# Optimization experiments

Measured on AMD Instinct MI355X. Metric: run time of the kernel, lower is better.

The kernel has to match this reference:

```python
import jax, jax.numpy as jnp
import numpy as np


def _quantum_act(x, act_w):
    # LearnedQuantumActivation, eval mode (no phase noise): softmax-weighted mix of 9 activations
    w = jax.nn.softmax(act_w)
    mish = x * jnp.tanh(jax.nn.softplus(x))
    return (w[0] * jax.nn.sigmoid(x) + w[1] * jax.nn.elu(x) + w[2] * jnp.tanh(x)
            + w[3] * jax.nn.relu(x) + w[4] * jax.nn.silu(x)
            + w[5] * jax.nn.gelu(x, approximate=False) + w[6] * jax.nn.selu(x)
            + w[7] * mish + w[8] * x)


def setup_inputs() -> dict:
    B, D, U, N = 1024, 1024, 2048, 4      # batch, input_dim, max_units, num_branches
    M, MD, O, H = 2048, 1024, 512, 64     # memory_size, memory_dim, output_dim, critic hidden
    key = jax.random.key(0)
    ks = jax.random.split(key, 16)
    g = lambda k, shape, s=0.02: jax.random.normal(k, shape, dtype=jnp.float32) * s
    return {
        "x": jax.random.normal(ks[0], (B, D), dtype=jnp.float32),
        "w": g(ks[1], (D, U, N)),
        "b": jnp.zeros((U, N), jnp.float32),
        "gate_w": g(ks[2], (D, N)), "gate_b": jnp.zeros((N,), jnp.float32),
        "act_w": jnp.ones((9,), jnp.float32),
        "mask": jnp.ones((U,), jnp.float32),          # neuron_mask, initial_units == max_units
        "mem": g(ks[3], (M, MD), 0.05),
        "att_w": g(ks[4], (U, M)), "att_b": jnp.zeros((M,), jnp.float32),
        "write_w": g(ks[5], (U, MD)), "write_b": jnp.zeros((MD,), jnp.float32),
        "update_gate": jnp.full((M,), 0.5, jnp.float32),
        "out_w": g(ks[6], (U, O)), "out_b": jnp.zeros((O,), jnp.float32),
        "cw1": g(ks[7], (MD, H // 2)), "cb1": jnp.zeros((H // 2,), jnp.float32),
        "cw2": g(ks[8], (O, H // 2)), "cb2": jnp.zeros((H // 2,), jnp.float32),
        "cw3": g(ks[9], (U, H // 2)), "cb3": jnp.zeros((H // 2,), jnp.float32),
        "cw4": g(ks[10], (3 * (H // 2), H)), "cb4": jnp.zeros((H,), jnp.float32),
        "cw5": g(ks[11], (H, 2)), "cb5": jnp.zeros((2,), jnp.float32),
        "meta_threshold": jnp.float32(0.5),
    }


def reference(x, w, b, gate_w, gate_b, act_w, mask, mem, att_w, att_b,
              write_w, write_b, update_gate, out_w, out_b,
              cw1, cb1, cw2, cb2, cw3, cb3, cw4, cb4, cw5, cb5, meta_threshold):
    # Dendritic plastic dense: per-branch projections mixed by a learned softmax branch gate
    pre = jnp.einsum('bi,iun->bun', x, w) + b               # (B, U, N)
    gate = jax.nn.softmax(x @ gate_w + gate_b, axis=-1)     # (B, N)
    hidden = _quantum_act(jnp.einsum('bun,bn->bu', pre, gate), act_w) * mask  # (B, U)
    # Episodic memory read + write (write is returned instead of in-place assign)
    read_att = jax.nn.softmax(hidden @ att_w + att_b, axis=-1)  # (B, M)
    read = read_att @ mem                                       # (B, MD)
    cand = jnp.tanh(hidden @ write_w + write_b)                 # (B, MD)
    u = (jnp.mean(read_att, axis=0) * update_gate)[:, None]     # (M, 1)
    new_mem = mem * (1.0 - u) + u * jnp.mean(cand, axis=0)      # (M, MD)
    # Prediction head
    preds = hidden @ out_w + out_b                              # (B, O)
    # Metacognitive critic gating
    mf = jax.nn.relu(read @ cw1 + cb1)
    pf = jax.nn.relu(preds @ cw2 + cb2)
    hf = jax.nn.relu(hidden @ cw3 + cb3)
    fused = jax.nn.relu(jnp.concatenate([mf, pf, hf], axis=-1) @ cw4 + cb4)
    outs = fused @ cw5 + cb5
    gating = jax.nn.sigmoid(outs[:, 0:1] - meta_threshold)
    return (preds * gating, new_mem)
```

## Files before the change

### kernel.cpp

```cpp
#include <hip/hip_runtime.h>
#include <hip/hip_bf16.h>
#include <math.h>

typedef __attribute__((ext_vector_type(4))) float f32x4;
typedef __attribute__((ext_vector_type(2))) float f32x2;
typedef __attribute__((ext_vector_type(8))) short s16x8;
typedef __attribute__((ext_vector_type(4))) short s16x4;
typedef __hip_bfloat16 bf16;

#define MB (1024ull*1024ull)
#define GATE_OFF    (0ull)
#define ACTW_OFF    (16ull*1024)
#define U_OFF       (20ull*1024)
#define CMEAN_OFF   (28ull*1024)
#define PART_OFF    (64ull*1024)
#define HIDDEN_OFF  (1ull*MB)
#define RATT_OFF    (5ull*MB)
#define CAND_OFF    (9ull*MB)
#define PREDS_OFF   (11ull*MB)
#define READ_OFF    (13ull*MB)
#define XBF_OFF     (17ull*MB)
#define WT_OFF      (19ull*MB)
#define CATT_OFF    (35ull*MB)
#define MEMT_OFF    (49ull*MB)
#define READ2_OFF   WT_OFF

__device__ __forceinline__ short f2bf_s(float f) {
    bf16 h = __float2bfloat16(f);
    return *reinterpret_cast<short*>(&h);
}

__device__ __forceinline__ void async_load16(const bf16* g, short* l) {
    __builtin_amdgcn_global_load_lds((const __attribute__((address_space(1))) void*)g,
                                     (__attribute__((address_space(3))) void*)l, 16, 0, 0);
}

__device__ __forceinline__ float fast_tanh(float x) {
    float e2x = __expf(2.f * x);
    return 1.f - 2.f / (e2x + 1.f);
}

__device__ __forceinline__ float qact(float x, const float* w) {
    float ex  = __expf(x);
    float r1  = 1.f / (1.f + ex);
    float sig = 1.f - r1;
    float em1 = ex - 1.f;
    float elu = x > 0.f ? x : em1;
    float e2x = ex * ex;
    float th  = 1.f - 2.f / (e2x + 1.f);
    float rel = fmaxf(x, 0.f);
    float silu = x * sig;
    float u   = 0.7978845608028654f * (x + 0.044715f * x * x * x);
    float e2u = __expf(2.f * u);
    float gel = x * (1.f - 1.f / (e2u + 1.f));
    float sel = 1.0507009873554805f * (x > 0.f ? x : 1.6732632423543772f * em1);
    float t   = 1.f + ex;
    float t2  = t * t;
    float mish = x * (1.f - 2.f / (t2 + 1.f));
    return w[0]*sig + w[1]*elu + w[2]*th + w[3]*rel + w[4]*silu
         + w[5]*gel + w[6]*sel + w[7]*mish + w[8]*x;
}

__device__ __forceinline__ void do_transpose(const float* __restrict__ in,
                                             bf16* __restrict__ out, int R, int C,
                                             int bx, int by, int t, short* tile) {
    int k0 = by*64, n0 = bx*64;
    int i = t & 31, half = t >> 5;
    #pragma unroll
    for (int r = 0; r < 8; r++) {
        int k = half + r*8;
        f32x2 v = *reinterpret_cast<const f32x2*>(&in[(size_t)(k0 + k)*C + n0 + i*2]);
        tile[(i*2 + 0)*66 + k] = f2bf_s(v[0]);
        tile[(i*2 + 1)*66 + k] = f2bf_s(v[1]);
    }
    __syncthreads();
    int kp = t & 31, nrow = t >> 5;
    #pragma unroll
    for (int jj = 0; jj < 8; jj++) {
        int n = nrow + jj*8;
        unsigned lo = (unsigned short)tile[n*66 + kp*2];
        unsigned hi = (unsigned short)tile[n*66 + kp*2 + 1];
        *reinterpret_cast<unsigned*>(&out[(size_t)(n0 + n)*R + k0 + kp*2]) = lo | (hi << 16);
    }
}

__global__ __launch_bounds__(256) void k_prepass(
        const float* __restrict__ x, bf16* __restrict__ xbf,
        const float* __restrict__ gw, const float* __restrict__ gb,
        const float* __restrict__ aw_in,
        float* __restrict__ gate, float* __restrict__ actw,
        const float* __restrict__ w_, bf16* __restrict__ wT,
        const float* __restrict__ att_w, const float* __restrict__ write_w,
        const float* __restrict__ out_w, bf16* __restrict__ catT,
        const float* __restrict__ mem, bf16* __restrict__ memT,
        float* __restrict__ zbase) {
    __shared__ short tile[64*66];
    int blk = blockIdx.x, t = threadIdx.x;
    if (blk < 2048) {
        do_transpose(w_, wT, 1024, 8192, blk & 127, blk >> 7, t, tile);
    } else if (blk < 3072) {
        int rel = blk - 2048;
        do_transpose(att_w, catT, 2048, 2048, rel & 31, rel >> 5, t, tile);
    } else if (blk < 3584) {
        int rel = blk - 3072;
        do_transpose(write_w, catT + 2048ull*2048, 2048, 1024, rel & 15, rel >> 4, t, tile);
    } else if (blk < 3840) {
        int rel = blk - 3584;
        do_transpose(out_w, catT + 3072ull*2048, 2048, 512, rel & 7, rel >> 3, t, tile);
    } else if (blk < 4352) {
        int rel = blk - 3840;
        do_transpose(mem, memT, 2048, 1024, rel & 15, rel >> 4, t, tile);
    } else if (blk < 5376) {
        int i = (blk - 4352)*256 + t;
        f32x4 v = ((const f32x4*)x)[i];
        s16x4 o;
        #pragma unroll
        for (int j = 0; j < 4; j++) o[j] = f2bf_s(v[j]);
        ((s16x4*)xbf)[i] = o;
        if (blk == 4352 && t == 64) {
            float a[9]; float m = -1e30f;
            for (int i2 = 0; i2 < 9; i2++) { a[i2] = aw_in[i2]; m = fmaxf(m, a[i2]); }
            float ss = 0.f;
            for (int i2 = 0; i2 < 9; i2++) { a[i2] = __expf(a[i2]-m); ss += a[i2]; }
            float inv = 1.f / ss;
            for (int i2 = 0; i2 < 9; i2++) actw[i2] = a[i2]*inv;
        }
    } else if (blk < 6400) {
        int b = blk - 5376, w = t >> 6, lane = t & 63;
        __shared__ float l[4];
        float s = 0.f;
        for (int k = lane; k < 1024; k += 64)
            s += x[(size_t)b*1024 + k] * gw[k*4 + w];
        #pragma unroll
        for (int off = 32; off; off >>= 1) s += __shfl_xor(s, off);
        if (lane == 0) l[w] = s + gb[w];
        __syncthreads();
        if (t == 0) {
            float m = fmaxf(fmaxf(l[0], l[1]), fmaxf(l[2], l[3]));
            float e0 = __expf(l[0]-m), e1 = __expf(l[1]-m), e2 = __expf(l[2]-m), e3 = __expf(l[3]-m);
            float inv = 1.f / (e0+e1+e2+e3);
            gate[b*4+0] = e0*inv; gate[b*4+1] = e1*inv;
            gate[b*4+2] = e2*inv; gate[b*4+3] = e3*inv;
        }
    } else {
        int idx = (blk - 6400)*256 + t;
        ((f32x4*)zbase)[idx] = (f32x4){0.f, 0.f, 0.f, 0.f};
    }
}

template <int TM>
union SMemT {
    struct { short a[3][TM*32]; short b[3][128*32]; } tl;
    float z[TM*32];
};

template <int MODE, int TM>
__device__ __forceinline__ void gemm_core(
        int bx, int by, int bz, SMemT<TM>& sm,
        const bf16* __restrict__ A, const bf16* __restrict__ Bt,
        int K, int lda, int ldb, int kOffset,
        const float* __restrict__ bias, const float* __restrict__ bias2,
        const float* __restrict__ bias3,
        float* __restrict__ outF, float* __restrict__ outF2,
        bf16* __restrict__ outH, bf16* __restrict__ outH2,
        const float* __restrict__ gate, const float* __restrict__ actw,
        const float* __restrict__ mask, int outStride) {
    constexpr int MI = TM / 32;
    int t = threadIdx.x, lane = t & 63;
    int rowBase = by * TM, colBase = bx * 128;
    int lm = lane & 15, lq = lane >> 4;
    int w = t >> 6;
    int qm = (w >> 1) * (TM/2), qn = (w & 1) * 64;

    A  += (size_t)kOffset * bz;
    Bt += (size_t)kOffset * bz;

    f32x4 acc[MI][4];
    #pragma unroll
    for (int i = 0; i < MI; i++)
        #pragma unroll
        for (int j = 0; j < 4; j++) acc[i][j] = (f32x4){0.f, 0.f, 0.f, 0.f};

    int cb0 = w*128 + lane, cb1 = cb0 + 64;
    int rb0 = cb0 >> 2, kb0 = ((cb0 & 3) ^ ((rb0 >> 1) & 3)) * 8;
    int rb1 = cb1 >> 2, kb1 = ((cb1 & 3) ^ ((rb1 >> 1) & 3)) * 8;
    int ca0 = (TM == 128) ? (w*128 + lane) : (w*64 + lane);
    int ra0 = ca0 >> 2, ka0 = ((ca0 & 3) ^ ((ra0 >> 1) & 3)) * 8;
    int ca1 = ca0 + 64;
    int ra1 = ca1 >> 2, ka1 = ((ca1 & 3) ^ ((ra1 >> 1) & 3)) * 8;

    auto issueLoads = [&](int k0, int ib) {
        short* bA = sm.tl.a[ib];
        short* bB = sm.tl.b[ib];
        async_load16(A + (size_t)(rowBase + ra0)*lda + k0 + ka0,
                     bA + ((TM == 128) ? w*1024 : w*512));
        if (TM == 128)
            async_load16(A + (size_t)(rowBase + ra1)*lda + k0 + ka1, bA + w*1024 + 512);
        async_load16(Bt + (size_t)(colBase + rb0)*ldb + k0 + kb0, bB + w*1024);
        async_load16(Bt + (size_t)(colBase + rb1)*ldb + k0 + kb1, bB + w*1024 + 512);
    };

    issueLoads(0, 0);
    if (32 < K) issueLoads(32, 1);
    int ib = 0;
    for (int k0 = 0; k0 < K; k0 += 32) {
        if (k0 + 32 < K) {
            if (TM == 128) asm volatile("s_waitcnt vmcnt(4)" ::: "memory");
            else           asm volatile("s_waitcnt vmcnt(3)" ::: "memory");
        } else {
            asm volatile("s_waitcnt vmcnt(0)" ::: "memory");
        }
        __builtin_amdgcn_sched_barrier(0);
        __builtin_amdgcn_s_barrier();
        __builtin_amdgcn_sched_barrier(0);
        int ibn = ib + 2; if (ibn >= 3) ibn -= 3;
        if (k0 + 64 < K) issueLoads(k0 + 64, ibn);
        const short* cA = sm.tl.a[ib];
        const short* cB = sm.tl.b[ib];
        s16x8 af[MI], bfr[4];
        #pragma unroll
        for (int mi = 0; mi < MI; mi++) {
            int r = qm + mi*16 + lm;
            af[mi] = *reinterpret_cast<const s16x8*>(cA + r*32 + ((lq ^ ((r >> 1) & 3)) * 8));
        }
        #pragma unroll
        for (int ni = 0; ni < 4; ni++) {
            int r = qn + ni*16 + lm;
            bfr[ni] = *reinterpret_cast<const s16x8*>(cB + r*32 + ((lq ^ ((r >> 1) & 3)) * 8));
        }
        #pragma unroll
        for (int mi = 0; mi < MI; mi++)
            #pragma unroll
            for (int ni = 0; ni < 4; ni++)
                acc[mi][ni] = __builtin_amdgcn_mfma_f32_16x16x32_bf16(af[mi], bfr[ni], acc[mi][ni], 0, 0, 0);
        ib += 1; if (ib >= 3) ib = 0;
    }

    if (MODE == 4) {
        __syncthreads();
        #pragma unroll
        for (int mi = 0; mi < MI; mi++) {
            int rowl0 = qm + mi*16 + lq*4;
            #pragma unroll
            for (int ni = 0; ni < 4; ni++) {
                int col = colBase + qn + ni*16 + lm;
                int n = col & 3;
                float bb = bias[col];
                f32x4 v = acc[mi][ni];
                #pragma unroll
                for (int r = 0; r < 4; r++) v[r] = (v[r] + bb) * gate[(rowBase + rowl0 + r)*4 + n];
                #pragma unroll
                for (int r = 0; r < 4; r++) v[r] += __shfl_xor(v[r], 1);
                #pragma unroll
                for (int r = 0; r < 4; r++) v[r] += __shfl_xor(v[r], 2);
                if ((lane & 3) == 0) {
                    int ul = ((w & 1) << 4) + ni*4 + (lm >> 2);
                    #pragma unroll
                    for (int r = 0; r < 4; r++)
                        sm.z[(rowl0 + r)*32 + ul] = v[r];
                }
            }
        }
        __syncthreads();
        float aw[9];
        #pragma unroll
        for (int i = 0; i < 9; i++) aw[i] = actw[i];
        int u0 = colBase >> 2;
        #pragma unroll
        for (int i = 0; i < TM/8; i++) {
            int idx = t + i*256;
            int row = idx >> 5, ul = idx & 31;
            int ug = u0 + ul;
            float zz = sm.z[idx];
            outH[(size_t)(rowBase + row)*outStride + ug] = __float2bfloat16(qact(zz, aw) * mask[ug]);
        }
    } else if (MODE == 5) {
        #pragma unroll
        for (int mi = 0; mi < MI; mi++) {
            int row0 = rowBase + qm + mi*16 + lq*4;
            #pragma unroll
            for (int ni = 0; ni < 4; ni++) {
                int col = colBase + qn + ni*16 + lm;
                if (col < 2048) {
                    float bb = bias[col];
                    #pragma unroll
                    for (int r = 0; r < 4; r++)
                        outH[(size_t)(row0 + r)*2048 + col] = __float2bfloat16(acc[mi][ni][r] + bb);
                } else if (col < 3072) {
                    int c = col - 2048;
                    float bb = bias2[c];
                    #pragma unroll
                    for (int r = 0; r < 4; r++)
                        outH2[(size_t)(row0 + r)*1024 + c] = __float2bfloat16(fast_tanh(acc[mi][ni][r] + bb));
                } else {
                    int c = col - 3072;
                    float bb = bias3[c];
                    #pragma unroll
                    for (int r = 0; r < 4; r++)
                        outF[(size_t)(row0 + r)*512 + c] = acc[mi][ni][r] + bb;
                }
            }
        }
    } else {
        float* of = bz ? (outF2 + (size_t)(bz - 1) * 1048576) : outF;
        #pragma unroll
        for (int mi = 0; mi < MI; mi++) {
            int row0 = rowBase + qm + mi*16 + lq*4;
            #pragma unroll
            for (int ni = 0; ni < 4; ni++) {
                int col = colBase + qn + ni*16 + lm;
                #pragma unroll
                for (int r = 0; r < 4; r++)
                    of[(size_t)(row0 + r)*outStride + col] = acc[mi][ni][r];
            }
        }
    }
}

template <int MODE, int TM>
__global__ __launch_bounds__(256, 2) void gemm_bt(
        const bf16* __restrict__ A, const bf16* __restrict__ Bt,
        int K, int lda, int ldb, int kOffset,
        const float* __restrict__ bias, const float* __restrict__ bias2,
        const float* __restrict__ bias3,
        float* __restrict__ outF, float* __restrict__ outF2,
        bf16* __restrict__ outH, bf16* __restrict__ outH2,
        const float* __restrict__ gate, const float* __restrict__ actw,
        const float* __restrict__ mask, int outStride) {
    __shared__ __align__(16) SMemT<TM> sm;
    gemm_core<MODE, TM>(blockIdx.x, blockIdx.y, blockIdx.z, sm,
                        A, Bt, K, lda, ldb, kOffset, bias, bias2, bias3,
                        outF, outF2, outH, outH2, gate, actw, mask, outStride);
}

__global__ __launch_bounds__(256) void k_softmax(bf16* __restrict__ ratt) {
    int b = blockIdx.x, t = threadIdx.x, w = t >> 6, lane = t & 63;
    __shared__ float red[8];
    bf16* row = ratt + (size_t)b*2048;
    float v[8];
    float mx = -1e30f;
    #pragma unroll
    for (int j = 0; j < 8; j++) {
        v[j] = __bfloat162float(row[t + j*256]);
        mx = fmaxf(mx, v[j]);
    }
    #pragma unroll
    for (int off = 32; off; off >>= 1) mx = fmaxf(mx, __shfl_xor(mx, off));
    if (lane == 0) red[w] = mx;
    __syncthreads();
    mx = fmaxf(fmaxf(red[0], red[1]), fmaxf(red[2], red[3]));
    float s = 0.f;
    #pragma unroll
    for (int j = 0; j < 8; j++) { v[j] = __expf(v[j] - mx); s += v[j]; }
    #pragma unroll
    for (int off = 32; off; off >>= 1) s += __shfl_xor(s, off);
    if (lane == 0) red[4 + w] = s;
    __syncthreads();
    float inv = 1.f / (red[4] + red[5] + red[6] + red[7]);
    #pragma unroll
    for (int j = 0; j < 8; j++)
        row[t + j*256] = __float2bfloat16(v[j] * inv);
}

__global__ __launch_bounds__(256, 2) void k_g5x(
        const bf16* __restrict__ ratt, const bf16* __restrict__ memT,
        const bf16* __restrict__ cand,
        float* __restrict__ readv, float* __restrict__ readv2,
        const float* __restrict__ update_gate,
        float* __restrict__ u, float* __restrict__ cmean) {
    __shared__ __align__(16) SMemT<64> sm;
    int bid = blockIdx.x, t = threadIdx.x;
    if (bid < 512) {
        int bx = bid & 7, by = (bid >> 3) & 15, bz = bid >> 7;
        gemm_core<3, 64>(bx, by, bz, sm, ratt, memT, 512, 2048, 2048, 512,
                         nullptr, nullptr, nullptr, readv, readv2, nullptr, nullptr,
                         nullptr, nullptr, nullptr, 1024);
    } else {
        int rel = bid - 512;
        int ct = rel % 12, rc = rel / 12;
        int col = ct*256 + t;
        const bf16* src; int stride, c;
        if (ct < 8) { src = ratt; stride = 2048; c = col; }
        else        { src = cand; stride = 1024; c = col - 2048; }
        float s = 0.f;
        int r0 = rc*128;
        for (int r2 = 0; r2 < 128; r2++)
            s += __bfloat162float(src[(size_t)(r0 + r2)*stride + c]);
        if (ct < 8) atomicAdd(&u[col], s * (update_gate[col] * (1.f/1024.f)));
        else        atomicAdd(&cmean[col - 2048], s * (1.f/1024.f));
    }
}

__global__ __launch_bounds__(256) void k_fin(
        const float* __restrict__ readv, const float* __restrict__ readv2,
        const float* __restrict__ preds, const bf16* __restrict__ hidden,
        const float* cw1, const float* cb1, const float* cw2, const float* cb2,
        const float* cw3, const float* cb3, const float* cw4, const float* cb4,
        const float* cw5, const float* cb5, const float* thr,
        float* __restrict__ out0,
        const float* __restrict__ mem, const float* __restrict__ u,
        const float* __restrict__ cmean, float* __restrict__ out1) {
    __shared__ __align__(16) float sx[2*1024];
    __shared__ __align__(16) float sp[2*512];
    __shared__ __align__(16) short sh[2*2048];
    __shared__ __align__(16) f32x4 part[2][32][8];
    __shared__ float feat[2][96];
    __shared__ float fused[2][64];
    __shared__ float gsh[2];
    int bid = blockIdx.x, t = threadIdx.x;
    if (bid >= 512) {
        int idx = (bid - 512)*256 + t;
        int m = idx >> 8, d4 = idx & 255;
        float um = u[m];
        f32x4 m4 = ((const f32x4*)mem)[idx];
        f32x4 c4 = ((const f32x4*)cmean)[d4];
        f32x4 o;
        #pragma unroll
        for (int j = 0; j < 4; j++) o[j] = m4[j] * (1.f - um) + um * c4[j];
        ((f32x4*)out1)[idx] = o;
        return;
    }
    int b0 = bid * 2;
    int j4 = t & 7, kg = t >> 3;

    {
        const f32x4* r0 = (const f32x4*)(readv  + (size_t)b0*1024);
        const f32x4* r1 = (const f32x4*)(readv2 + (size_t)b0*1024);
        const f32x4* r2 = (const f32x4*)(readv2 + 1048576 + (size_t)b0*1024);
        const f32x4* r3 = (const f32x4*)(readv2 + 2097152 + (size_t)b0*1024);
        ((f32x4*)sx)[t]       = r0[t] + r1[t] + r2[t] + r3[t];
        ((f32x4*)sx)[t + 256] = r0[t + 256] + r1[t + 256] + r2[t + 256] + r3[t + 256];
    }
    ((f32x4*)sp)[t]       = ((const f32x4*)(preds + (size_t)b0*512))[t];
    ((s16x8*)sh)[t]       = ((const s16x8*)(hidden + (size_t)b0*2048))[t];
    ((s16x8*)sh)[t + 256] = ((const s16x8*)(hidden + (size_t)b0*2048))[t + 256];
    __syncthreads();

    {
        const f32x4* wv = (const f32x4*)cw1;
        f32x4 a0 = (f32x4){0,0,0,0}, a1 = (f32x4){0,0,0,0};
        int k0 = kg*32;
        #pragma unroll 4
        for (int k = k0; k < k0 + 32; k++) {
            f32x4 wq = wv[k*8 + j4];
            a0 += sx[k] * wq;
            a1 += sx[1024 + k] * wq;
        }
        part[0][kg][j4] = a0; part[1][kg][j4] = a1;
    }
    __syncthreads();
    if (t < 64) {
        int r = t >> 5, f = t & 31;
        float s = 0.f;
        #pragma unroll
        for (int i = 0; i < 32; i++) s += part[r][i][f >> 2][f & 3];
        feat[r][f] = fmaxf(s + cb1[f], 0.f);
    }
    __syncthreads();
    {
        const f32x4* wv = (const f32x4*)cw2;
        f32x4 a0 = (f32x4){0,0,0,0}, a1 = (f32x4){0,0,0,0};
        int k0 = kg*16;
        #pragma unroll 4
        for (int k = k0; k < k0 + 16; k++) {
            f32x4 wq = wv[k*8 + j4];
            a0 += sp[k] * wq;
            a1 += sp[512 + k] * wq;
        }
        part[0][kg][j4] = a0; part[1][kg][j4] = a1;
    }
    __syncthreads();
    if (t < 64) {
        int r = t >> 5, f = t & 31;
        float s = 0.f;
        #pragma unroll
        for (int i = 0; i < 32; i++) s += part[r][i][f >> 2][f & 3];
        feat[r][32 + f] = fmaxf(s + cb2[f], 0.f);
    }
    __syncthreads();
    {
        const f32x4* wv = (const f32x4*)cw3;
        f32x4 a0 = (f32x4){0,0,0,0}, a1 = (f32x4){0,0,0,0};
        int k0 = kg*64;
        #pragma unroll 4
        for (int k = k0; k < k0 + 64; k++) {
            f32x4 wq = wv[k*8 + j4];
            float h0 = __bfloat162float(*reinterpret_cast<const bf16*>(&sh[k]));
            float h1 = __bfloat162float(*reinterpret_cast<const bf16*>(&sh[2048 + k]));
            a0 += h0 * wq;
            a1 += h1 * wq;
        }
        part[0][kg][j4] = a0; part[1][kg][j4] = a1;
    }
    __syncthreads();
    if (t < 64) {
        int r = t >> 5, f = t & 31;
        float s = 0.f;
        #pragma unroll
        for (int i = 0; i < 32; i++) s += part[r][i][f >> 2][f & 3];
        feat[r][64 + f] = fmaxf(s + cb3[f], 0.f);
    }
    __syncthreads();
    if (t < 128) {
        int r = t >> 6, uu = t & 63;
        float s = 0.f;
        #pragma unroll 8
        for (int k = 0; k < 96; k++) s += feat[r][k] * cw4[k*64 + uu];
        fused[r][uu] = fmaxf(s + cb4[uu], 0.f);
    }
    __syncthreads();
    if (t < 128) {
        int r = t >> 6, lane = t & 63;
        float v = fused[r][lane] * cw5[lane*2];
        #pragma unroll
        for (int off = 32; off; off >>= 1) v += __shfl_xor(v, off);
        if (lane == 0)
            gsh[r] = 1.f / (1.f + __expf(-(v + cb5[0] - thr[0])));
    }
    __syncthreads();
    #pragma unroll
    for (int idx = t; idx < 1024; idx += 256) {
        int r = idx >> 9, o = idx & 511;
        out0[(size_t)(b0 + r)*512 + o] = sp[r*512 + o] * gsh[r];
    }
}

extern "C" void kernel_launch(void* const* d_in, const int* in_sizes, int n_in,
                              void* d_out, int out_size, void* d_ws, size_t ws_size,
                              hipStream_t stream) {
    const float* x        = (const float*)d_in[0];
    const float* w_       = (const float*)d_in[1];
    const float* b_bias   = (const float*)d_in[2];
    const float* gate_w   = (const float*)d_in[3];
    const float* gate_b   = (const float*)d_in[4];
    const float* act_w    = (const float*)d_in[5];
    const float* mask     = (const float*)d_in[6];
    const float* mem      = (const float*)d_in[7];
    const float* att_w    = (const float*)d_in[8];
    const float* att_b    = (const float*)d_in[9];
    const float* write_w  = (const float*)d_in[10];
    const float* write_b  = (const float*)d_in[11];
    const float* upd_gate = (const float*)d_in[12];
    const float* out_w    = (const float*)d_in[13];
    const float* out_b    = (const float*)d_in[14];
    const float* cw1 = (const float*)d_in[15]; const float* cb1 = (const float*)d_in[16];
    const float* cw2 = (const float*)d_in[17]; const float* cb2 = (const float*)d_in[18];
    const float* cw3 = (const float*)d_in[19]; const float* cb3 = (const float*)d_in[20];
    const float* cw4 = (const float*)d_in[21]; const float* cb4 = (const float*)d_in[22];
    const float* cw5 = (const float*)d_in[23]; const float* cb5 = (const float*)d_in[24];
    const float* thr = (const float*)d_in[25];

    char* ws = (char*)d_ws;
    float* gate   = (float*)(ws + GATE_OFF);
    float* actw   = (float*)(ws + ACTW_OFF);
    float* uvec   = (float*)(ws + U_OFF);
    float* cmean  = (float*)(ws + CMEAN_OFF);
    bf16*  hidden = (bf16*)(ws + HIDDEN_OFF);
    bf16*  ratt   = (bf16*)(ws + RATT_OFF);
    bf16*  cand   = (bf16*)(ws + CAND_OFF);
    float* preds  = (float*)(ws + PREDS_OFF);
    float* readv  = (float*)(ws + READ_OFF);
    float* readv2 = (float*)(ws + READ2_OFF);
    bf16*  xbf    = (bf16*)(ws + XBF_OFF);
    bf16*  wT     = (bf16*)(ws + WT_OFF);
    bf16*  catT   = (bf16*)(ws + CATT_OFF);
    bf16*  memT   = (bf16*)(ws + MEMT_OFF);

    float* out0 = (float*)d_out;
    float* out1 = out0 + 1024*512;

    k_prepass<<<6403, 256, 0, stream>>>(x, xbf, gate_w, gate_b, act_w, gate, actw,
                                        w_, wT, att_w, write_w, out_w, catT, mem, memT,
                                        uvec);

    gemm_bt<4, 128><<<dim3(64, 8), 256, 0, stream>>>(xbf, wT, 1024, 1024, 1024, 0,
        b_bias, nullptr, nullptr, nullptr, nullptr, hidden, nullptr, gate, actw, mask, 2048);

    gemm_bt<5, 64><<<dim3(28, 16), 256, 0, stream>>>(hidden, catT, 2048, 2048, 2048, 0,
        att_b, write_b, out_b, preds, nullptr, ratt, cand, nullptr, nullptr, nullptr, 0);
    k_softmax<<<1024, 256, 0, stream>>>(ratt);
    k_g5x<<<608, 256, 0, stream>>>(ratt, memT, cand, readv, readv2, upd_gate, uvec, cmean);

    k_fin<<<2560, 256, 0, stream>>>(readv, readv2, preds, hidden,
        cw1, cb1, cw2, cb2, cw3, cb3, cw4, cb4, cw5, cb5, thr, out0,
        mem, uvec, cmean, out1);
}
```

Measured before the change: 265.4 us.

## Merge stages into three persistent-style kernels synchronized by global atomic counters

Replaces six kernel launches with three merged kernels. Inside each one, later block ranges spin-wait on a global atomic counter that earlier blocks increment on completion. The attention, write, output and memory transposes are moved behind the first GEMM so they can overlap with it. The aim is to remove launch gaps and inter-kernel drains. It relies on block dispatch order to avoid deadlock and adds spin-wait polling and a memset.

```diff
diff --git a/kernel.cpp b/kernel.cpp
--- a/kernel.cpp
+++ b/kernel.cpp
@@ -13,7 +13,6 @@
 #define ACTW_OFF    (16ull*1024)
 #define U_OFF       (20ull*1024)
 #define CMEAN_OFF   (28ull*1024)
-#define PART_OFF    (64ull*1024)
 #define HIDDEN_OFF  (1ull*MB)
 #define RATT_OFF    (5ull*MB)
 #define CAND_OFF    (9ull*MB)
@@ -23,6 +22,7 @@
 #define WT_OFF      (19ull*MB)
 #define CATT_OFF    (35ull*MB)
 #define MEMT_OFF    (49ull*MB)
+#define CTR_OFF     (60ull*MB)
 #define READ2_OFF   WT_OFF
 
 __device__ __forceinline__ short f2bf_s(float f) {
@@ -38,6 +38,18 @@
 __device__ __forceinline__ float fast_tanh(float x) {
     float e2x = __expf(2.f * x);
     return 1.f - 2.f / (e2x + 1.f);
+}
+
+__device__ __forceinline__ void bump_ctr(unsigned* c) {
+    __syncthreads();
+    if (threadIdx.x == 0) { __threadfence(); atomicAdd(c, 1u); }
+}
+__device__ __forceinline__ void wait_ctr(unsigned* c, unsigned tgt) {
+    if (threadIdx.x == 0) {
+        while (atomicAdd(c, 0u) < tgt) __builtin_amdgcn_s_sleep(8);
+        __threadfence();
+    }
+    __syncthreads();
 }
 
 __device__ __forceinline__ float qact(float x, const float* w) {
@@ -84,74 +96,11 @@
     }
 }
 
-__global__ __launch_bounds__(256) void k_prepass(
-        const float* __restrict__ x, bf16* __restrict__ xbf,
-        const float* __restrict__ gw, const float* __restrict__ gb,
-        const float* __restrict__ aw_in,
-        float* __restrict__ gate, float* __restrict__ actw,
-        const float* __restrict__ w_, bf16* __restrict__ wT,
-        const float* __restrict__ att_w, const float* __restrict__ write_w,
-        const float* __restrict__ out_w, bf16* __restrict__ catT,
-        const float* __restrict__ mem, bf16* __restrict__ memT,
-        float* __restrict__ zbase) {
-    __shared__ short tile[64*66];
-    int blk = blockIdx.x, t = threadIdx.x;
-    if (blk < 2048) {
-        do_transpose(w_, wT, 1024, 8192, blk & 127, blk >> 7, t, tile);
-    } else if (blk < 3072) {
-        int rel = blk - 2048;
-        do_transpose(att_w, catT, 2048, 2048, rel & 31, rel >> 5, t, tile);
-    } else if (blk < 3584) {
-        int rel = blk - 3072;
-        do_transpose(write_w, catT + 2048ull*2048, 2048, 1024, rel & 15, rel >> 4, t, tile);
-    } else if (blk < 3840) {
-        int rel = blk - 3584;
-        do_transpose(out_w, catT + 3072ull*2048, 2048, 512, rel & 7, rel >> 3, t, tile);
-    } else if (blk < 4352) {
-        int rel = blk - 3840;
-        do_transpose(mem, memT, 2048, 1024, rel & 15, rel >> 4, t, tile);
-    } else if (blk < 5376) {
-        int i = (blk - 4352)*256 + t;
-        f32x4 v = ((const f32x4*)x)[i];
-        s16x4 o;
-        #pragma unroll
-        for (int j = 0; j < 4; j++) o[j] = f2bf_s(v[j]);
-        ((s16x4*)xbf)[i] = o;
-        if (blk == 4352 && t == 64) {
-            float a[9]; float m = -1e30f;
-            for (int i2 = 0; i2 < 9; i2++) { a[i2] = aw_in[i2]; m = fmaxf(m, a[i2]); }
-            float ss = 0.f;
-            for (int i2 = 0; i2 < 9; i2++) { a[i2] = __expf(a[i2]-m); ss += a[i2]; }
-            float inv = 1.f / ss;
-            for (int i2 = 0; i2 < 9; i2++) actw[i2] = a[i2]*inv;
-        }
-    } else if (blk < 6400) {
-        int b = blk - 5376, w = t >> 6, lane = t & 63;
-        __shared__ float l[4];
-        float s = 0.f;
-        for (int k = lane; k < 1024; k += 64)
-            s += x[(size_t)b*1024 + k] * gw[k*4 + w];
-        #pragma unroll
-        for (int off = 32; off; off >>= 1) s += __shfl_xor(s, off);
-        if (lane == 0) l[w] = s + gb[w];
-        __syncthreads();
-        if (t == 0) {
-            float m = fmaxf(fmaxf(l[0], l[1]), fmaxf(l[2], l[3]));
-            float e0 = __expf(l[0]-m), e1 = __expf(l[1]-m), e2 = __expf(l[2]-m), e3 = __expf(l[3]-m);
-            float inv = 1.f / (e0+e1+e2+e3);
-            gate[b*4+0] = e0*inv; gate[b*4+1] = e1*inv;
-            gate[b*4+2] = e2*inv; gate[b*4+3] = e3*inv;
-        }
-    } else {
-        int idx = (blk - 6400)*256 + t;
-        ((f32x4*)zbase)[idx] = (f32x4){0.f, 0.f, 0.f, 0.f};
-    }
-}
-
 template <int TM>
 union SMemT {
     struct { short a[3][TM*32]; short b[3][128*32]; } tl;
     float z[TM*32];
+    short tr[64*66];
 };
 
 template <int MODE, int TM>
@@ -317,26 +266,86 @@
     }
 }
 
-template <int MODE, int TM>
-__global__ __launch_bounds__(256, 2) void gemm_bt(
-        const bf16* __restrict__ A, const bf16* __restrict__ Bt,
-        int K, int lda, int ldb, int kOffset,
-        const float* __restrict__ bias, const float* __restrict__ bias2,
-        const float* __restrict__ bias3,
-        float* __restrict__ outF, float* __restrict__ outF2,
-        bf16* __restrict__ outH, bf16* __restrict__ outH2,
-        const float* __restrict__ gate, const float* __restrict__ actw,
-        const float* __restrict__ mask, int outStride) {
-    __shared__ __align__(16) SMemT<TM> sm;
-    gemm_core<MODE, TM>(blockIdx.x, blockIdx.y, blockIdx.z, sm,
-                        A, Bt, K, lda, ldb, kOffset, bias, bias2, bias3,
-                        outF, outF2, outH, outH2, gate, actw, mask, outStride);
-}
-
-__global__ __launch_bounds__(256) void k_softmax(bf16* __restrict__ ratt) {
-    int b = blockIdx.x, t = threadIdx.x, w = t >> 6, lane = t & 63;
-    __shared__ float red[8];
-    bf16* row = ratt + (size_t)b*2048;
+__global__ __launch_bounds__(256, 2) void k_mega1(
+        const float* __restrict__ x, bf16* __restrict__ xbf,
+        const float* __restrict__ gw, const float* __restrict__ gb,
+        const float* __restrict__ aw_in,
+        float* __restrict__ gate, float* __restrict__ actw,
+        const float* __restrict__ w_, bf16* __restrict__ wT,
+        const float* __restrict__ att_w, const float* __restrict__ write_w,
+        const float* __restrict__ out_w, bf16* __restrict__ catT,
+        const float* __restrict__ mem, bf16* __restrict__ memT,
+        float* __restrict__ zbase,
+        const float* __restrict__ bias, bf16* __restrict__ hidden,
+        const float* __restrict__ mask, unsigned* __restrict__ ctr1) {
+    __shared__ __align__(16) SMemT<128> sm;
+    int bid = blockIdx.x, t = threadIdx.x;
+    if (bid < 4099) {
+        if (bid < 2048) {
+            do_transpose(w_, wT, 1024, 8192, bid & 127, bid >> 7, t, sm.tr);
+        } else if (bid < 3072) {
+            int i = (bid - 2048)*256 + t;
+            f32x4 v = ((const f32x4*)x)[i];
+            s16x4 o;
+            #pragma unroll
+            for (int j = 0; j < 4; j++) o[j] = f2bf_s(v[j]);
+            ((s16x4*)xbf)[i] = o;
+            if (bid == 2048 && t == 64) {
+                float a[9]; float m = -1e30f;
+                for (int i2 = 0; i2 < 9; i2++) { a[i2] = aw_in[i2]; m = fmaxf(m, a[i2]); }
+                float ss = 0.f;
+                for (int i2 = 0; i2 < 9; i2++) { a[i2] = __expf(a[i2]-m); ss += a[i2]; }
+                float inv = 1.f / ss;
+                for (int i2 = 0; i2 < 9; i2++) actw[i2] = a[i2]*inv;
+            }
+        } else if (bid < 4096) {
+            int b = bid - 3072, w = t >> 6, lane = t & 63;
+            float* l = (float*)&sm;
+            float s = 0.f;
+            for (int k = lane; k < 1024; k += 64)
+                s += x[(size_t)b*1024 + k] * gw[k*4 + w];
+            #pragma unroll
+            for (int off = 32; off; off >>= 1) s += __shfl_xor(s, off);
+            if (lane == 0) l[w] = s + gb[w];
+            __syncthreads();
+            if (t == 0) {
+                float m = fmaxf(fmaxf(l[0], l[1]), fmaxf(l[2], l[3]));
+                float e0 = __expf(l[0]-m), e1 = __expf(l[1]-m), e2 = __expf(l[2]-m), e3 = __expf(l[3]-m);
+                float inv = 1.f / (e0+e1+e2+e3);
+                gate[b*4+0] = e0*inv; gate[b*4+1] = e1*inv;
+                gate[b*4+2] = e2*inv; gate[b*4+3] = e3*inv;
+            }
+        } else {
+            int idx = (bid - 4096)*256 + t;
+            ((f32x4*)zbase)[idx] = (f32x4){0.f, 0.f, 0.f, 0.f};
+        }
+        bump_ctr(ctr1);
+    } else if (bid < 4611) {
+        int c = bid - 4099;
+        wait_ctr(ctr1, 4099u);
+        gemm_core<4, 128>(c & 63, c >> 6, 0, sm, xbf, wT, 1024, 1024, 1024, 0,
+                          bias, nullptr, nullptr, nullptr, nullptr, hidden, nullptr,
+                          gate, actw, mask, 2048);
+    } else {
+        int rel = bid - 4611;
+        if (rel < 1024) {
+            do_transpose(att_w, catT, 2048, 2048, rel & 31, rel >> 5, t, sm.tr);
+        } else if (rel < 1536) {
+            rel -= 1024;
+            do_transpose(write_w, catT + 2048ull*2048, 2048, 1024, rel & 15, rel >> 4, t, sm.tr);
+        } else if (rel < 1792) {
+            rel -= 1536;
+            do_transpose(out_w, catT + 3072ull*2048, 2048, 512, rel & 7, rel >> 3, t, sm.tr);
+        } else {
+            rel -= 1792;
+            do_transpose(mem, memT, 2048, 1024, rel & 15, rel >> 4, t, sm.tr);
+        }
+    }
+}
+
+__device__ __forceinline__ void softmax_row(bf16* __restrict__ row, int t, float* red) {
+    int w = t >> 6, lane = t & 63;
+    __syncthreads();
     float v[8];
     float mx = -1e30f;
     #pragma unroll
@@ -362,20 +371,61 @@
         row[t + j*256] = __float2bfloat16(v[j] * inv);
 }
 
-__global__ __launch_bounds__(256, 2) void k_g5x(
+__global__ __launch_bounds__(256, 2) void k_mega2(
+        const bf16* __restrict__ hidden, const bf16* __restrict__ catT,
+        const float* __restrict__ att_b, const float* __restrict__ write_b,
+        const float* __restrict__ out_b,
+        float* __restrict__ preds, bf16* __restrict__ ratt, bf16* __restrict__ cand,
+        unsigned* __restrict__ ctr2) {
+    __shared__ __align__(16) SMemT<64> sm;
+    int bid = blockIdx.x, t = threadIdx.x;
+    if (bid < 448) {
+        gemm_core<5, 64>(bid % 28, bid / 28, 0, sm, hidden, catT, 2048, 2048, 2048, 0,
+                         att_b, write_b, out_b, preds, nullptr, ratt, cand,
+                         nullptr, nullptr, nullptr, 0);
+        bump_ctr(ctr2);
+    } else {
+        wait_ctr(ctr2, 448u);
+        int r0 = (bid - 448)*2;
+        float* red = (float*)&sm;
+        softmax_row(ratt + (size_t)r0*2048, t, red);
+        softmax_row(ratt + (size_t)(r0 + 1)*2048, t, red);
+    }
+}
+
+__global__ __launch_bounds__(256, 2) void k_mega3(
         const bf16* __restrict__ ratt, const bf16* __restrict__ memT,
         const bf16* __restrict__ cand,
         float* __restrict__ readv, float* __restrict__ readv2,
         const float* __restrict__ update_gate,
-        float* __restrict__ u, float* __restrict__ cmean) {
-    __shared__ __align__(16) SMemT<64> sm;
+        float* __restrict__ u, float* __restrict__ cmean,
+        const float* __restrict__ preds, const bf16* __restrict__ hidden,
+        const float* cw1, const float* cb1, const float* cw2, const float* cb2,
+        const float* cw3, const float* cb3, const float* cw4, const float* cb4,
+        const float* cw5, const float* cb5, const float* thr,
+        float* __restrict__ out0,
+        const float* __restrict__ mem, float* __restrict__ out1,
+        unsigned* __restrict__ ctr3) {
+    struct CriticSM {
+        float sx[2*1024];
+        float sp[2*512];
+        short sh[2*2048];
+        f32x4 part[2][32][8];
+        float feat[2][96];
+        float fused[2][64];
+        float gsh[2];
+    };
+    __shared__ __align__(16) union { SMemT<64> g; CriticSM c; } sm;
     int bid = blockIdx.x, t = threadIdx.x;
     if (bid < 512) {
         int bx = bid & 7, by = (bid >> 3) & 15, bz = bid >> 7;
-        gemm_core<3, 64>(bx, by, bz, sm, ratt, memT, 512, 2048, 2048, 512,
+        gemm_core<3, 64>(bx, by, bz, sm.g, ratt, memT, 512, 2048, 2048, 512,
                          nullptr, nullptr, nullptr, readv, readv2, nullptr, nullptr,
                          nullptr, nullptr, nullptr, 1024);
-    } else {
+        bump_ctr(ctr3);
+        return;
+    }
+    if (bid < 608) {
         int rel = bid - 512;
         int ct = rel % 12, rc = rel / 12;
         int col = ct*256 + t;
@@ -388,54 +438,40 @@
             s += __bfloat162float(src[(size_t)(r0 + r2)*stride + c]);
         if (ct < 8) atomicAdd(&u[col], s * (update_gate[col] * (1.f/1024.f)));
         else        atomicAdd(&cmean[col - 2048], s * (1.f/1024.f));
-    }
-}
-
-__global__ __launch_bounds__(256) void k_fin(
-        const float* __restrict__ readv, const float* __restrict__ readv2,
-        const float* __restrict__ preds, const bf16* __restrict__ hidden,
-        const float* cw1, const float* cb1, const float* cw2, const float* cb2,
-        const float* cw3, const float* cb3, const float* cw4, const float* cb4,
-        const float* cw5, const float* cb5, const float* thr,
-        float* __restrict__ out0,
-        const float* __restrict__ mem, const float* __restrict__ u,
-        const float* __restrict__ cmean, float* __restrict__ out1) {
-    __shared__ __align__(16) float sx[2*1024];
-    __shared__ __align__(16) float sp[2*512];
-    __shared__ __align__(16) short sh[2*2048];
-    __shared__ __align__(16) f32x4 part[2][32][8];
-    __shared__ float feat[2][96];
-    __shared__ float fused[2][64];
-    __shared__ float gsh[2];
-    int bid = blockIdx.x, t = threadIdx.x;
-    if (bid >= 512) {
-        int idx = (bid - 512)*256 + t;
-        int m = idx >> 8, d4 = idx & 255;
-        float um = u[m];
-        f32x4 m4 = ((const f32x4*)mem)[idx];
-        f32x4 c4 = ((const f32x4*)cmean)[d4];
-        f32x4 o;
-        #pragma unroll
-        for (int j = 0; j < 4; j++) o[j] = m4[j] * (1.f - um) + um * c4[j];
-        ((f32x4*)out1)[idx] = o;
+        bump_ctr(ctr3);
         return;
     }
-    int b0 = bid * 2;
+    wait_ctr(ctr3, 608u);
+    if (bid >= 1120) {
+        int nb = bid - 1120;
+        #pragma unroll
+        for (int i = 0; i < 8; i++) {
+            int idx = nb*2048 + i*256 + t;
+            int m = idx >> 8, d4 = idx & 255;
+            float um = u[m];
+            f32x4 m4 = ((const f32x4*)mem)[idx];
+            f32x4 c4 = ((const f32x4*)cmean)[d4];
+            f32x4 o;
+            #pragma unroll
+            for (int j = 0; j < 4; j++) o[j] = m4[j] * (1.f - um) + um * c4[j];
+            ((f32x4*)out1)[idx] = o;
+        }
+        return;
+    }
+    int b0 = (bid - 608) * 2;
     int j4 = t & 7, kg = t >> 3;
-
     {
         const f32x4* r0 = (const f32x4*)(readv  + (size_t)b0*1024);
         const f32x4* r1 = (const f32x4*)(readv2 + (size_t)b0*1024);
         const f32x4* r2 = (const f32x4*)(readv2 + 1048576 + (size_t)b0*1024);
         const f32x4* r3 = (const f32x4*)(readv2 + 2097152 + (size_t)b0*1024);
-        ((f32x4*)sx)[t]       = r0[t] + r1[t] + r2[t] + r3[t];
-        ((f32x4*)sx)[t + 256] = r0[t + 256] + r1[t + 256] + r2[t + 256] + r3[t + 256];
-    }
-    ((f32x4*)sp)[t]       = ((const f32x4*)(preds + (size_t)b0*512))[t];
-    ((s16x8*)sh)[t]       = ((const s16x8*)(hidden + (size_t)b0*2048))[t];
-    ((s16x8*)sh)[t + 256] = ((const s16x8*)(hidden + (size_t)b0*2048))[t + 256];
-    __syncthreads();
-
+        ((f32x4*)sm.c.sx)[t]       = r0[t] + r1[t] + r2[t] + r3[t];
+        ((f32x4*)sm.c.sx)[t + 256] = r0[t + 256] + r1[t + 256] + r2[t + 256] + r3[t + 256];
+    }
+    ((f32x4*)sm.c.sp)[t]       = ((const f32x4*)(preds + (size_t)b0*512))[t];
+    ((s16x8*)sm.c.sh)[t]       = ((const s16x8*)(hidden + (size_t)b0*2048))[t];
+    ((s16x8*)sm.c.sh)[t + 256] = ((const s16x8*)(hidden + (size_t)b0*2048))[t + 256];
+    __syncthreads();
     {
         const f32x4* wv = (const f32x4*)cw1;
         f32x4 a0 = (f32x4){0,0,0,0}, a1 = (f32x4){0,0,0,0};
@@ -443,18 +479,18 @@
         #pragma unroll 4
         for (int k = k0; k < k0 + 32; k++) {
             f32x4 wq = wv[k*8 + j4];
-            a0 += sx[k] * wq;
-            a1 += sx[1024 + k] * wq;
-        }
-        part[0][kg][j4] = a0; part[1][kg][j4] = a1;
+            a0 += sm.c.sx[k] * wq;
+            a1 += sm.c.sx[1024 + k] * wq;
+        }
+        sm.c.part[0][kg][j4] = a0; sm.c.part[1][kg][j4] = a1;
     }
     __syncthreads();
     if (t < 64) {
         int r = t >> 5, f = t & 31;
         float s = 0.f;
         #pragma unroll
-        for (int i = 0; i < 32; i++) s += part[r][i][f >> 2][f & 3];
-        feat[r][f] = fmaxf(s + cb1[f], 0.f);
+        for (int i = 0; i < 32; i++) s += sm.c.part[r][i][f >> 2][f & 3];
+        sm.c.feat[r][f] = fmaxf(s + cb1[f], 0.f);
     }
     __syncthreads();
     {
@@ -464,18 +500,18 @@
         #pragma unroll 4
         for (int k = k0; k < k0 + 16; k++) {
             f32x4 wq = wv[k*8 + j4];
-            a0 += sp[k] * wq;
-            a1 += sp[512 + k] * wq;
-        }
-        part[0][kg][j4] = a0; part[1][kg][j4] = a1;
+            a0 += sm.c.sp[k] * wq;
+            a1 += sm.c.sp[512 + k] * wq;
+        }
+        sm.c.part[0][kg][j4] = a0; sm.c.part[1][kg][j4] = a1;
     }
     __syncthreads();
     if (t < 64) {
         int r = t >> 5, f = t & 31;
         float s = 0.f;
         #pragma unroll
-        for (int i = 0; i < 32; i++) s += part[r][i][f >> 2][f & 3];
-        feat[r][32 + f] = fmaxf(s + cb2[f], 0.f);
+        for (int i = 0; i < 32; i++) s += sm.c.part[r][i][f >> 2][f & 3];
+        sm.c.feat[r][32 + f] = fmaxf(s + cb2[f], 0.f);
     }
     __syncthreads();
     {
@@ -485,43 +521,43 @@
         #pragma unroll 4
         for (int k = k0; k < k0 + 64; k++) {
             f32x4 wq = wv[k*8 + j4];
-            float h0 = __bfloat162float(*reinterpret_cast<const bf16*>(&sh[k]));
-            float h1 = __bfloat162float(*reinterpret_cast<const bf16*>(&sh[2048 + k]));
+            float h0 = __bfloat162float(*reinterpret_cast<const bf16*>(&sm.c.sh[k]));
+            float h1 = __bfloat162float(*reinterpret_cast<const bf16*>(&sm.c.sh[2048 + k]));
             a0 += h0 * wq;
             a1 += h1 * wq;
         }
-        part[0][kg][j4] = a0; part[1][kg][j4] = a1;
+        sm.c.part[0][kg][j4] = a0; sm.c.part[1][kg][j4] = a1;
     }
     __syncthreads();
     if (t < 64) {
         int r = t >> 5, f = t & 31;
         float s = 0.f;
         #pragma unroll
-        for (int i = 0; i < 32; i++) s += part[r][i][f >> 2][f & 3];
-        feat[r][64 + f] = fmaxf(s + cb3[f], 0.f);
+        for (int i = 0; i < 32; i++) s += sm.c.part[r][i][f >> 2][f & 3];
+        sm.c.feat[r][64 + f] = fmaxf(s + cb3[f], 0.f);
     }
     __syncthreads();
     if (t < 128) {
         int r = t >> 6, uu = t & 63;
         float s = 0.f;
         #pragma unroll 8
-        for (int k = 0; k < 96; k++) s += feat[r][k] * cw4[k*64 + uu];
-        fused[r][uu] = fmaxf(s + cb4[uu], 0.f);
+        for (int k = 0; k < 96; k++) s += sm.c.feat[r][k] * cw4[k*64 + uu];
+        sm.c.fused[r][uu] = fmaxf(s + cb4[uu], 0.f);
     }
     __syncthreads();
     if (t < 128) {
         int r = t >> 6, lane = t & 63;
-        float v = fused[r][lane] * cw5[lane*2];
+        float v = sm.c.fused[r][lane] * cw5[lane*2];
         #pragma unroll
         for (int off = 32; off; off >>= 1) v += __shfl_xor(v, off);
         if (lane == 0)
-            gsh[r] = 1.f / (1.f + __expf(-(v + cb5[0] - thr[0])));
+            sm.c.gsh[r] = 1.f / (1.f + __expf(-(v + cb5[0] - thr[0])));
     }
     __syncthreads();
     #pragma unroll
     for (int idx = t; idx < 1024; idx += 256) {
         int r = idx >> 9, o = idx & 511;
-        out0[(size_t)(b0 + r)*512 + o] = sp[r*512 + o] * gsh[r];
+        out0[(size_t)(b0 + r)*512 + o] = sm.c.sp[r*512 + o] * sm.c.gsh[r];
     }
 }
 
@@ -565,23 +601,22 @@
     bf16*  wT     = (bf16*)(ws + WT_OFF);
     bf16*  catT   = (bf16*)(ws + CATT_OFF);
     bf16*  memT   = (bf16*)(ws + MEMT_OFF);
+    unsigned* ctrs = (unsigned*)(ws + CTR_OFF);
 
     float* out0 = (float*)d_out;
     float* out1 = out0 + 1024*512;
 
-    k_prepass<<<6403, 256, 0, stream>>>(x, xbf, gate_w, gate_b, act_w, gate, actw,
-                                        w_, wT, att_w, write_w, out_w, catT, mem, memT,
-                                        uvec);
-
-    gemm_bt<4, 128><<<dim3(64, 8), 256, 0, stream>>>(xbf, wT, 1024, 1024, 1024, 0,
-        b_bias, nullptr, nullptr, nullptr, nullptr, hidden, nullptr, gate, actw, mask, 2048);
-
-    gemm_bt<5, 64><<<dim3(28, 16), 256, 0, stream>>>(hidden, catT, 2048, 2048, 2048, 0,
-        att_b, write_b, out_b, preds, nullptr, ratt, cand, nullptr, nullptr, nullptr, 0);
-    k_softmax<<<1024, 256, 0, stream>>>(ratt);
-    k_g5x<<<608, 256, 0, stream>>>(ratt, memT, cand, readv, readv2, upd_gate, uvec, cmean);
-
-    k_fin<<<2560, 256, 0, stream>>>(readv, readv2, preds, hidden,
-        cw1, cb1, cw2, cb2, cw3, cb3, cw4, cb4, cw5, cb5, thr, out0,
-        mem, uvec, cmean, out1);
-}
+    hipMemsetAsync(ctrs, 0, 256, stream);
+
+    k_mega1<<<6915, 256, 0, stream>>>(x, xbf, gate_w, gate_b, act_w, gate, actw,
+                                      w_, wT, att_w, write_w, out_w, catT, mem, memT,
+                                      uvec, b_bias, hidden, mask, ctrs + 0);
+
+    k_mega2<<<960, 256, 0, stream>>>(hidden, catT, att_b, write_b, out_b,
+                                     preds, ratt, cand, ctrs + 1);
+
+    k_mega3<<<1376, 256, 0, stream>>>(ratt, memT, cand, readv, readv2, upd_gate,
+                                      uvec, cmean, preds, hidden,
+                                      cw1, cb1, cw2, cb2, cw3, cb3, cw4, cb4, cw5, cb5,
+                                      thr, out0, mem, out1, ctrs + 2);
+}
```

New measurement: 582.7 us. 120% more time.
